# Performance work log

Hardware: AMD Instinct MI355X
Metric: run time of the kernel (lower is better)

## Reference

```python
import jax, jax.numpy as jnp
import numpy as np

B, S, D, H = 2, 2048, 1024, 16
DH = D // H
EPS = 1e-5


def _ln(x, g, b):
    m = jnp.mean(x, axis=-1, keepdims=True)
    v = jnp.mean((x - m) ** 2, axis=-1, keepdims=True)
    return (x - m) * jax.lax.rsqrt(v + EPS) * g + b


def setup_inputs() -> dict:
    key = jax.random.key(0)
    ks = jax.random.split(key, 16)
    w = lambda k, shp: jax.random.normal(k, shp, jnp.float32) * 0.02
    return {
        "x": jax.random.normal(ks[0], (B, S, D), jnp.float32),
        # semantic preprocessor: Linear(D,2D) -> ReLU -> Linear(2D,D), residual + LN
        "pW1": w(ks[1], (D, 2 * D)), "pb1": jnp.zeros((2 * D,), jnp.float32),
        "pW2": w(ks[2], (2 * D, D)), "pb2": jnp.zeros((D,), jnp.float32),
        "gp": jnp.ones((D,), jnp.float32), "bp": jnp.zeros((D,), jnp.float32),
        # multi-head attention projections
        "Wq": w(ks[3], (D, D)), "bq": jnp.zeros((D,), jnp.float32),
        "Wk": w(ks[4], (D, D)), "bk": jnp.zeros((D,), jnp.float32),
        "Wv": w(ks[5], (D, D)), "bv": jnp.zeros((D,), jnp.float32),
        "Wo": w(ks[6], (D, D)), "bo": jnp.zeros((D,), jnp.float32),
        "g1": jnp.ones((D,), jnp.float32), "b1": jnp.zeros((D,), jnp.float32),
        # FFN: Linear(D,4D) -> ReLU -> Linear(4D,D)
        "Wf1": w(ks[7], (D, 4 * D)), "bf1": jnp.zeros((4 * D,), jnp.float32),
        "Wf2": w(ks[8], (4 * D, D)), "bf2": jnp.zeros((D,), jnp.float32),
        "g2": jnp.ones((D,), jnp.float32), "b2": jnp.zeros((D,), jnp.float32),
    }


def reference(x, pW1, pb1, pW2, pb2, gp, bp,
              Wq, bq, Wk, bk, Wv, bv, Wo, bo, g1, b1,
              Wf1, bf1, Wf2, bf2, g2, b2):
    # specialized 'semantic' preprocessor (dropout = identity in eval)
    h = jax.nn.relu(x @ pW1 + pb1) @ pW2 + pb2
    s = _ln(x + h, gp, bp)                       # [B,S,D]
    # naive multi-head attention
    q = (s @ Wq + bq).reshape(B, S, H, DH)
    k = (s @ Wk + bk).reshape(B, S, H, DH)
    v = (s @ Wv + bv).reshape(B, S, H, DH)
    scores = jnp.einsum("bqhd,bkhd->bhqk", q, k) / np.sqrt(DH).astype(np.float32)
    attn = jax.nn.softmax(scores, axis=-1)       # [B,H,S,S]
    ctx = jnp.einsum("bhqk,bkhd->bqhd", attn, v).reshape(B, S, D)
    attn_out = ctx @ Wo + bo
    y = _ln(s + attn_out, g1, b1)
    # FFN (dropouts = identity)
    f = jax.nn.relu(y @ Wf1 + bf1) @ Wf2 + bf2
    return _ln(y + f, g2, b2)
```

## Files before the change

kernel.cpp:

```cpp
#include <hip/hip_runtime.h>
#include <cstdint>
#include <cstddef>

typedef _Float16 f16;
typedef _Float16 f16x8 __attribute__((ext_vector_type(8)));
typedef _Float16 f16x4 __attribute__((ext_vector_type(4)));
typedef float    f32x4 __attribute__((ext_vector_type(4)));
typedef float    f32x16 __attribute__((ext_vector_type(16)));
typedef unsigned int uint2v __attribute__((ext_vector_type(2)));

#define MFMA16(a,b,c) __builtin_amdgcn_mfma_f32_16x16x32_f16(a, b, c, 0, 0, 0)
#define MFMA32(a,b,c) __builtin_amdgcn_mfma_f32_32x32x16_f16(a, b, c, 0, 0, 0)

static __device__ __forceinline__ void gload_lds16(const void* g, void* l) {
  __builtin_amdgcn_global_load_lds(
      (const __attribute__((address_space(1))) unsigned int*)g,
      (__attribute__((address_space(3))) unsigned int*)l, 16, 0, 0);
}

static __device__ __forceinline__ int pkh(float a, float b) {
  auto t = __builtin_amdgcn_cvt_pkrtz(a, b);
  return __builtin_bit_cast(int, t);
}

static __device__ __forceinline__ float ex2(float x) {
  return __builtin_amdgcn_exp2f(x);
}

static __device__ __forceinline__ uint2v pswap(int a, int b) {
  return __builtin_amdgcn_permlane32_swap((unsigned)a, (unsigned)b, false, false);
}
static __device__ __forceinline__ float xhalf_max(float x) {
  uint2v r = pswap(__builtin_bit_cast(int, x), __builtin_bit_cast(int, x));
  return fmaxf(__builtin_bit_cast(float, r.x), __builtin_bit_cast(float, r.y));
}
static __device__ __forceinline__ float f3(float a, float b, float c) {
  return fmaxf(fmaxf(a, b), c);
}

static __device__ __forceinline__ void wtrans_blk(float (*tile)[33],
                                                  const float* __restrict__ W,
                                                  f16* __restrict__ Wt,
                                                  int K, int N, int gx,
                                                  float scale, int lb) {
  const int n0 = (lb % gx) * 32, k0 = (lb / gx) * 32;
  const int c = threadIdx.x & 31, r = threadIdx.x >> 5;
#pragma unroll
  for (int i = 0; i < 4; i++) {
    int row = r + i * 8;
    tile[row][c] = W[(size_t)(k0 + row) * N + n0 + c];
  }
  __syncthreads();
#pragma unroll
  for (int i = 0; i < 4; i++) {
    int row = r + i * 8;
    Wt[(size_t)(n0 + row) * K + k0 + c] = (f16)(tile[c][row] * scale);
  }
}

__global__ __launch_bounds__(256)
void prep_kernel(const float* __restrict__ x, f16* __restrict__ xb,
                 const float* __restrict__ pW1, f16* __restrict__ wtP1,
                 const float* __restrict__ pW2, f16* __restrict__ wtP2,
                 const float* __restrict__ Wq,  f16* __restrict__ wtQ,
                 const float* __restrict__ Wk,  f16* __restrict__ wtK,
                 const float* __restrict__ Wv,  f16* __restrict__ wtV,
                 const float* __restrict__ Wo,  f16* __restrict__ wtO,
                 const float* __restrict__ Wf1, f16* __restrict__ wtF1,
                 const float* __restrict__ Wf2, f16* __restrict__ wtF2,
                 const float* __restrict__ bq, const float* __restrict__ bk,
                 const float* __restrict__ bv, float* __restrict__ bqkv) {
  __shared__ float tile[32][33];
  int b = blockIdx.x;
  if (b < 4096) {
    int i = b * 256 + threadIdx.x;
    float4 v = ((const float4*)x)[i];
    f16x4 h;
    h[0] = (f16)v.x; h[1] = (f16)v.y; h[2] = (f16)v.z; h[3] = (f16)v.w;
    *(f16x4*)(xb + (size_t)i * 4) = h;
    return;
  }
  b -= 4096;
  if (b < 2048) { wtrans_blk(tile, pW1, wtP1, 1024, 2048, 64, 1.f, b); return; }
  b -= 2048;
  if (b < 2048) { wtrans_blk(tile, pW2, wtP2, 2048, 1024, 32, 1.f, b); return; }
  b -= 2048;
  if (b < 1024) { wtrans_blk(tile, Wq, wtQ, 1024, 1024, 32, 0.18033688f, b); return; }
  b -= 1024;
  if (b < 1024) { wtrans_blk(tile, Wk, wtK, 1024, 1024, 32, 1.f, b); return; }
  b -= 1024;
  if (b < 1024) { wtrans_blk(tile, Wv, wtV, 1024, 1024, 32, 1.f, b); return; }
  b -= 1024;
  if (b < 1024) { wtrans_blk(tile, Wo, wtO, 1024, 1024, 32, 1.f, b); return; }
  b -= 1024;
  if (b < 4096) { wtrans_blk(tile, Wf1, wtF1, 1024, 4096, 128, 1.f, b); return; }
  b -= 4096;
  if (b < 4096) { wtrans_blk(tile, Wf2, wtF2, 4096, 1024, 32, 1.f, b); return; }
  b -= 4096;
  {
    int i = b * 256 + threadIdx.x;
    if (i < 1024)       bqkv[i] = bq[i] * 0.18033688f;
    else if (i < 2048)  bqkv[i] = bk[i - 1024];
    else if (i < 3072)  bqkv[i] = bv[i - 2048];
  }
}

template <int MODE>
__global__ __launch_bounds__(256, 2)
void gemm_kernel(const f16* __restrict__ A, const f16* __restrict__ W,
                 const float* __restrict__ bias, void* __restrict__ out,
                 f16* __restrict__ vt, int N, int K, int gx) {
  __shared__ __align__(16) f16 lsA[128 * 64];
  __shared__ __align__(16) f16 lsB[128 * 64];
  const int tid  = threadIdx.x;
  const int lane = tid & 63;
  const int wid  = tid >> 6;
  const int frow = lane & 15;
  const int kgrp = lane >> 4;
  const int wmBase = (wid >> 1) * 64;
  const int wnBase = (wid & 1) * 64;

  const int bid = blockIdx.x;
  const int xcd = bid & 7, slot = bid >> 3;
  const int bm = (xcd << 2) + slot / gx;
  const int bn = slot % gx;

  const f32x4 zero4 = {0.f, 0.f, 0.f, 0.f};
  f32x4 acc[4][4];
#pragma unroll
  for (int i = 0; i < 4; i++)
#pragma unroll
    for (int j = 0; j < 4; j++) acc[i][j] = zero4;

  const f16* aSrc[4]; int lOffA[4];
  const f16* bSrc[4];
#pragma unroll
  for (int i = 0; i < 4; i++) {
    int c_lin = i * 256 + wid * 64 + lane;
    int row = c_lin >> 3;
    int ch  = (c_lin & 7) ^ (row & 7);
    aSrc[i] = A + (size_t)(bm * 128 + row) * K + ch * 8;
    bSrc[i] = W + (size_t)(bn * 128 + row) * K + ch * 8;
    lOffA[i] = (i * 256 + wid * 64) * 8;
  }

  const int nk = K >> 6;
  for (int ks = 0; ks < nk; ++ks) {
#pragma unroll
    for (int i = 0; i < 4; i++) gload_lds16(aSrc[i] + ks * 64, &lsA[lOffA[i]]);
#pragma unroll
    for (int i = 0; i < 4; i++) gload_lds16(bSrc[i] + ks * 64, &lsB[lOffA[i]]);
    __syncthreads();
#pragma unroll
    for (int kk = 0; kk < 2; kk++) {
      f16x8 af[4], bf[4];
#pragma unroll
      for (int i = 0; i < 4; i++) {
        int row = wmBase + i * 16 + frow;
        af[i] = *(const f16x8*)&lsA[row * 64 + (((kk * 4 + kgrp) ^ (row & 7)) << 3)];
      }
#pragma unroll
      for (int j = 0; j < 4; j++) {
        int row = wnBase + j * 16 + frow;
        bf[j] = *(const f16x8*)&lsB[row * 64 + (((kk * 4 + kgrp) ^ (row & 7)) << 3)];
      }
#pragma unroll
      for (int i = 0; i < 4; i++)
#pragma unroll
        for (int j = 0; j < 4; j++) acc[i][j] = MFMA16(af[i], bf[j], acc[i][j]);
    }
    __syncthreads();
  }

#pragma unroll
  for (int j = 0; j < 4; j++) {
    const int col = bn * 128 + wnBase + j * 16 + frow;
    const float bb = bias[col];
#pragma unroll
    for (int i = 0; i < 4; i++) {
      const int row0 = bm * 128 + wmBase + i * 16 + kgrp * 4;
      if (MODE == 3 && col >= 2048) {
        const int vcol = col - 2048;
        const int bh = (row0 >> 11) * 16 + (vcol >> 6);
        const int d  = vcol & 63;
        const int kv = row0 & 2047;
        f16x4 pk;
#pragma unroll
        for (int r = 0; r < 4; r++) pk[r] = (f16)(acc[i][j][r] + bb);
        *(f16x4*)(vt + ((size_t)bh * 64 + d) * 2048 + kv) = pk;
      } else {
#pragma unroll
        for (int r = 0; r < 4; r++) {
          float v = acc[i][j][r] + bb;
          if (MODE == 1) v = fmaxf(v, 0.f);
          ((f16*)out)[(size_t)(row0 + r) * N + col] = (f16)v;
        }
      }
    }
  }
}

__global__ __launch_bounds__(256, 2)
void gemm_splitk(const f16* __restrict__ A, const f16* __restrict__ W,
                 f16* __restrict__ outp, int K) {
  __shared__ __align__(16) f16 lsA[128 * 64];
  __shared__ __align__(16) f16 lsB[128 * 64];
  const int tid  = threadIdx.x;
  const int lane = tid & 63;
  const int wid  = tid >> 6;
  const int frow = lane & 15;
  const int kgrp = lane >> 4;
  const int wmBase = (wid >> 1) * 64;
  const int wnBase = (wid & 1) * 64;

  const int bid = blockIdx.x;
  const int xcd = bid & 7, slot = bid >> 3;
  const int q = slot >> 3, bn = slot & 7;
  const int bmkp = xcd * 8 + q;
  const int bm = bmkp >> 1, kp = bmkp & 1;
  const int Kh = K >> 1;
  const f16* Ab = A + kp * Kh;
  const f16* Wb = W + kp * Kh;

  const f32x4 zero4 = {0.f, 0.f, 0.f, 0.f};
  f32x4 acc[4][4];
#pragma unroll
  for (int i = 0; i < 4; i++)
#pragma unroll
    for (int j = 0; j < 4; j++) acc[i][j] = zero4;

  const f16* aSrc[4]; const f16* bSrc[4]; int lOff[4];
#pragma unroll
  for (int i = 0; i < 4; i++) {
    int c_lin = i * 256 + wid * 64 + lane;
    int row = c_lin >> 3;
    int ch  = (c_lin & 7) ^ (row & 7);
    aSrc[i] = Ab + (size_t)(bm * 128 + row) * K + ch * 8;
    bSrc[i] = Wb + (size_t)(bn * 128 + row) * K + ch * 8;
    lOff[i] = (i * 256 + wid * 64) * 8;
  }

  const int nk = Kh >> 6;
  for (int ks = 0; ks < nk; ++ks) {
#pragma unroll
    for (int i = 0; i < 4; i++) gload_lds16(aSrc[i] + ks * 64, &lsA[lOff[i]]);
#pragma unroll
    for (int i = 0; i < 4; i++) gload_lds16(bSrc[i] + ks * 64, &lsB[lOff[i]]);
    __syncthreads();
#pragma unroll
    for (int kk = 0; kk < 2; kk++) {
      f16x8 af[4], bf[4];
#pragma unroll
      for (int i = 0; i < 4; i++) {
        int row = wmBase + i * 16 + frow;
        af[i] = *(const f16x8*)&lsA[row * 64 + (((kk * 4 + kgrp) ^ (row & 7)) << 3)];
      }
#pragma unroll
      for (int j = 0; j < 4; j++) {
        int row = wnBase + j * 16 + frow;
        bf[j] = *(const f16x8*)&lsB[row * 64 + (((kk * 4 + kgrp) ^ (row & 7)) << 3)];
      }
#pragma unroll
      for (int i = 0; i < 4; i++)
#pragma unroll
        for (int j = 0; j < 4; j++) acc[i][j] = MFMA16(af[i], bf[j], acc[i][j]);
    }
    __syncthreads();
  }

  f16* op = outp + (size_t)kp * 4096 * 1024;
#pragma unroll
  for (int j = 0; j < 4; j++) {
    const int col = bn * 128 + wnBase + j * 16 + frow;
#pragma unroll
    for (int i = 0; i < 4; i++) {
      const int row0 = bm * 128 + wmBase + i * 16 + kgrp * 4;
#pragma unroll
      for (int r = 0; r < 4; r++)
        op[(size_t)(row0 + r) * 1024 + col] = (f16)acc[i][j][r];
    }
  }
}

__global__ __launch_bounds__(256)
void ln_res2(const f16* __restrict__ p, const f16* __restrict__ res,
             const float* __restrict__ bias, const float* __restrict__ g,
             const float* __restrict__ be, float* __restrict__ of,
             f16* __restrict__ ob) {
  const int row = blockIdx.x, t = threadIdx.x;
  const size_t off = (size_t)row * 1024 + t * 4;
  const f16x4 a = *(const f16x4*)(p + off);
  const f16x4 b = *(const f16x4*)(p + (size_t)4096 * 1024 + off);
  const f16x4 rr = *(const f16x4*)(res + off);
  const float4 bb = ((const float4*)bias)[t];
  float v0 = (float)a[0] + (float)b[0] + bb.x + (float)rr[0];
  float v1 = (float)a[1] + (float)b[1] + bb.y + (float)rr[1];
  float v2 = (float)a[2] + (float)b[2] + bb.z + (float)rr[2];
  float v3 = (float)a[3] + (float)b[3] + bb.w + (float)rr[3];
  float s = v0 + v1 + v2 + v3;
  float q = v0 * v0 + v1 * v1 + v2 * v2 + v3 * v3;
#pragma unroll
  for (int o = 1; o < 64; o <<= 1) {
    s += __shfl_xor(s, o);
    q += __shfl_xor(q, o);
  }
  __shared__ float ss[4], sq[4];
  if ((t & 63) == 0) { ss[t >> 6] = s; sq[t >> 6] = q; }
  __syncthreads();
  s = ss[0] + ss[1] + ss[2] + ss[3];
  q = sq[0] + sq[1] + sq[2] + sq[3];
  const float mean = s * (1.f / 1024.f);
  const float var  = q * (1.f / 1024.f) - mean * mean;
  const float rstd = rsqrtf(var + 1e-5f);
  const float4 gv = ((const float4*)g)[t];
  const float4 bv = ((const float4*)be)[t];
  float4 ov;
  ov.x = (v0 - mean) * rstd * gv.x + bv.x;
  ov.y = (v1 - mean) * rstd * gv.y + bv.y;
  ov.z = (v2 - mean) * rstd * gv.z + bv.z;
  ov.w = (v3 - mean) * rstd * gv.w + bv.w;
  if (of) ((float4*)(of + (size_t)row * 1024))[t] = ov;
  if (ob) {
    f16x4 hv;
    hv[0] = (f16)ov.x; hv[1] = (f16)ov.y; hv[2] = (f16)ov.z; hv[3] = (f16)ov.w;
    *(f16x4*)(ob + off) = hv;
  }
}

__global__ __launch_bounds__(256, 4)
void attn_kernel(const f16* __restrict__ Qp, const f16* __restrict__ Kp,
                 const f16* __restrict__ Vt, f16* __restrict__ opart,
                 float* __restrict__ Lbuf, int ldq) {
  __shared__ __align__(16) f16 lsKb[2 * 64 * 64];
  __shared__ __align__(16) f16 lsVb[2 * 64 * 64];
  const int tid = threadIdx.x, lane = tid & 63, wid = tid >> 6;
  const int qcol = lane & 31;
  const int hi = lane >> 5;
  const int bid = blockIdx.x;
  const int idx = bid >> 3;
  const int bh = ((bid & 7) << 2) | (idx & 3);
  const int rest = idx >> 2;
  const int part = rest & 1;
  const int qt = rest >> 1;
  const int b = bh >> 4, h = bh & 15;
  const size_t rb = (size_t)b * 2048;
  const int hc = h * 64;
  const int kv0 = part * 1024;
  const int qrow = qt * 128 + wid * 32 + qcol;

  f16x8 qf[4];
  {
    const f16* qp = Qp + (rb + qrow) * ldq + hc;
#pragma unroll
    for (int kc = 0; kc < 4; kc++) qf[kc] = *(const f16x8*)(qp + kc * 16 + hi * 8);
  }
  f16x8 ones;
#pragma unroll
  for (int i = 0; i < 8; i++) ones[i] = (f16)1.0f;

  f32x16 ot0, ot1, lacc;
#pragma unroll
  for (int i = 0; i < 16; i++) { ot0[i] = 0.f; ot1[i] = 0.f; lacc[i] = 0.f; }
  float mrun = -1e30f;

  const f16 *kS0, *kS1, *vS0, *vS1;
  int off0, off1;
  {
    int c0 = wid * 64 + lane;
    int r0 = c0 >> 3, ch0 = (c0 & 7) ^ (r0 & 7);
    int c1 = 256 + wid * 64 + lane;
    int r1 = c1 >> 3, ch1 = (c1 & 7) ^ (r1 & 7);
    kS0 = Kp + (rb + kv0 + r0) * ldq + hc + ch0 * 8;
    kS1 = Kp + (rb + kv0 + r1) * ldq + hc + ch1 * 8;
    const f16* vbase = Vt + (size_t)bh * 64 * 2048 + kv0;
    vS0 = vbase + (size_t)r0 * 2048 + ch0 * 8;
    vS1 = vbase + (size_t)r1 * 2048 + ch1 * 8;
    off0 = (wid * 64) * 8;
    off1 = (256 + wid * 64) * 8;
  }

#define ASTAGE(T, PB)                                                    \
  {                                                                      \
    f16* kd = lsKb + (PB) * 4096;                                        \
    f16* vd = lsVb + (PB) * 4096;                                        \
    const size_t ko = (size_t)(T) * 64 * ldq;                            \
    const size_t vo = (size_t)(T) * 64;                                  \
    gload_lds16(kS0 + ko, kd + off0);                                    \
    gload_lds16(kS1 + ko, kd + off1);                                    \
    gload_lds16(vS0 + vo, vd + off0);                                    \
    gload_lds16(vS1 + vo, vd + off1);                                    \
  }

  ASTAGE(0, 0);
  asm volatile("s_waitcnt vmcnt(0)" ::: "memory");
  __builtin_amdgcn_s_barrier();

  for (int kt = 0; kt < 16; ++kt) {
    const int cur = kt & 1;
    if (kt < 15) ASTAGE(kt + 1, cur ^ 1);
    const f16* kb = lsKb + cur * 4096;
    const f16* vb = lsVb + cur * 4096;

    f32x16 s0, s1;
#pragma unroll
    for (int i = 0; i < 16; i++) { s0[i] = 0.f; s1[i] = 0.f; }
    const int kr0 = qcol, kr1 = 32 + qcol;
    __builtin_amdgcn_s_setprio(1);
#pragma unroll
    for (int kc = 0; kc < 4; kc++) {
      f16x8 a0 = *(const f16x8*)&kb[kr0 * 64 + (((kc * 2 + hi) ^ (kr0 & 7)) << 3)];
      f16x8 a1 = *(const f16x8*)&kb[kr1 * 64 + (((kc * 2 + hi) ^ (kr1 & 7)) << 3)];
      s0 = MFMA32(a0, qf[kc], s0);
      s1 = MFMA32(a1, qf[kc], s1);
    }
    __builtin_amdgcn_s_setprio(0);

    float t10[11];
#pragma unroll
    for (int r = 0; r < 10; r++) {
      float e0 = (3 * r + 0 < 16) ? s0[(3 * r + 0) & 15] : s1[(3 * r + 0) & 15];
      float e1 = (3 * r + 1 < 16) ? s0[(3 * r + 1) & 15] : s1[(3 * r + 1) & 15];
      float e2 = (3 * r + 2 < 16) ? s0[(3 * r + 2) & 15] : s1[(3 * r + 2) & 15];
      t10[r] = f3(e0, e1, e2);
    }
    t10[10] = fmaxf(s1[14], s1[15]);
    float p0 = f3(t10[0], t10[1], t10[2]);
    float p1 = f3(t10[3], t10[4], t10[5]);
    float p2 = f3(t10[6], t10[7], t10[8]);
    float p3 = fmaxf(t10[9], t10[10]);
    float pmax = xhalf_max(fmaxf(fmaxf(p0, p1), fmaxf(p2, p3)));
    if (__any(pmax > mrun + 11.54f)) {
      float mn = fmaxf(mrun, pmax);
      float fac = ex2(mrun - mn);
      mrun = mn;
#pragma unroll
      for (int i = 0; i < 16; i++) {
        ot0[i] *= fac; ot1[i] *= fac; lacc[i] *= fac;
      }
    }
#pragma unroll
    for (int r = 0; r < 16; r++) {
      s0[r] = ex2(s0[r] - mrun);
      s1[r] = ex2(s1[r] - mrun);
    }

#pragma unroll
    for (int st = 0; st < 2; ++st) {
#pragma unroll
      for (int c0 = 0; c0 < 2; c0++) {
        const int c8 = c0 * 8;
        int a0, a1, b0, b1;
        if (st == 0) {
          a0 = pkh(s0[c8 + 0], s0[c8 + 1]); a1 = pkh(s0[c8 + 2], s0[c8 + 3]);
          b0 = pkh(s0[c8 + 4], s0[c8 + 5]); b1 = pkh(s0[c8 + 6], s0[c8 + 7]);
        } else {
          a0 = pkh(s1[c8 + 0], s1[c8 + 1]); a1 = pkh(s1[c8 + 2], s1[c8 + 3]);
          b0 = pkh(s1[c8 + 4], s1[c8 + 5]); b1 = pkh(s1[c8 + 6], s1[c8 + 7]);
        }
        uint2v r0 = pswap(a0, b0);
        uint2v r1 = pswap(a1, b1);
        int4 wv;
        wv.x = (int)r0.x; wv.y = (int)r1.x; wv.z = (int)r0.y; wv.w = (int)r1.y;
        f16x8 pfrag = __builtin_bit_cast(f16x8, wv);
        const int ch = st * 4 + c0 * 2 + hi;
        const int vr0 = qcol, vr1 = 32 + qcol;
        f16x8 av0 = *(const f16x8*)&vb[vr0 * 64 + ((ch ^ (vr0 & 7)) << 3)];
        f16x8 av1 = *(const f16x8*)&vb[vr1 * 64 + ((ch ^ (vr1 & 7)) << 3)];
        __builtin_amdgcn_s_setprio(1);
        ot0 = MFMA32(av0, pfrag, ot0);
        ot1 = MFMA32(av1, pfrag, ot1);
        lacc = MFMA32(ones, pfrag, lacc);
        __builtin_amdgcn_s_setprio(0);
      }
    }
    asm volatile("s_waitcnt vmcnt(0)" ::: "memory");
    __builtin_amdgcn_s_barrier();
  }
#undef ASTAGE

  const float lfin = lacc[0];
  const float rinv = 1.f / lfin;
  const size_t pbase = ((size_t)part * 32 + bh) * 2048 + qrow;
  f16* pp = opart + pbase * 64;
#pragma unroll
  for (int rr = 0; rr < 16; rr += 2) {
    const int d = (rr & 3) + 8 * (rr >> 2) + 4 * hi;
    *(int*)(pp + d)      = pkh(ot0[rr] * rinv, ot0[rr + 1] * rinv);
    *(int*)(pp + 32 + d) = pkh(ot1[rr] * rinv, ot1[rr + 1] * rinv);
  }
  if (hi == 0) Lbuf[pbase] = mrun + __builtin_amdgcn_logf(lfin);
}

__global__ __launch_bounds__(256)
void combine_kernel(const f16* __restrict__ opart, const float* __restrict__ Lbuf,
                    f16* __restrict__ ctx) {
  const int bid = blockIdx.x;
  const int bh = bid >> 5, qblk = bid & 31;
  const int t = threadIdx.x;
  const int q = qblk * 64 + (t >> 2);
  const int dp = (t & 3) * 16;
  const size_t base = (size_t)bh * 2048 + q;
  const size_t p1o = (size_t)32 * 2048;
  const float L0 = Lbuf[base];
  const float L1 = Lbuf[p1o + base];
  const float L = fmaxf(L0, L1);
  float w0 = ex2(L0 - L), w1 = ex2(L1 - L);
  const float rs = 1.f / (w0 + w1);
  w0 *= rs; w1 *= rs;
  const f16* p0 = opart + base * 64 + dp;
  const f16* p1 = opart + (p1o + base) * 64 + dp;
  f16x8 a0 = *(const f16x8*)p0, a1 = *(const f16x8*)(p0 + 8);
  f16x8 c0 = *(const f16x8*)p1, c1 = *(const f16x8*)(p1 + 8);
  f16x8 o0, o1;
#pragma unroll
  for (int j = 0; j < 8; j++) {
    o0[j] = (f16)(w0 * (float)a0[j] + w1 * (float)c0[j]);
    o1[j] = (f16)(w0 * (float)a1[j] + w1 * (float)c1[j]);
  }
  const int b = bh >> 4, h = bh & 15;
  f16* op = ctx + ((size_t)b * 2048 + q) * 1024 + h * 64 + dp;
  *(f16x8*)op = o0;
  *(f16x8*)(op + 8) = o1;
}

extern "C" void kernel_launch(void* const* d_in, const int* in_sizes, int n_in,
                              void* d_out, int out_size, void* d_ws, size_t ws_size,
                              hipStream_t stream) {
  const float* x   = (const float*)d_in[0];
  const float* pW1 = (const float*)d_in[1];
  const float* pb1 = (const float*)d_in[2];
  const float* pW2 = (const float*)d_in[3];
  const float* pb2 = (const float*)d_in[4];
  const float* gp  = (const float*)d_in[5];
  const float* bp  = (const float*)d_in[6];
  const float* Wq  = (const float*)d_in[7];
  const float* bq  = (const float*)d_in[8];
  const float* Wk  = (const float*)d_in[9];
  const float* bk  = (const float*)d_in[10];
  const float* Wv  = (const float*)d_in[11];
  const float* bv  = (const float*)d_in[12];
  const float* Wo  = (const float*)d_in[13];
  const float* bo  = (const float*)d_in[14];
  const float* g1  = (const float*)d_in[15];
  const float* b1  = (const float*)d_in[16];
  const float* Wf1 = (const float*)d_in[17];
  const float* bf1 = (const float*)d_in[18];
  const float* Wf2 = (const float*)d_in[19];
  const float* bf2 = (const float*)d_in[20];
  const float* g2  = (const float*)d_in[21];
  const float* b2  = (const float*)d_in[22];

  char* ws = (char*)d_ws;
  const size_t MB = 1024 * 1024;
  if (ws_size < 121 * MB) return;

  f16*   wtP1 = (f16*)(ws);
  f16*   wtP2 = (f16*)(ws + 4 * MB);
  f16*   wtQ  = (f16*)(ws + 8 * MB);
  f16*   wtO  = (f16*)(ws + 14 * MB);
  f16*   wtF1 = (f16*)(ws + 16 * MB);
  f16*   wtF2 = (f16*)(ws + 24 * MB);
  f16*   big  = (f16*)(ws + 32 * MB);
  f16*   xb   = (f16*)(ws + 64 * MB);
  f16*   sb   = (f16*)(ws + 72 * MB);
  f16*   ybuf = (f16*)(ws + 80 * MB);
  f16*   ctx  = (f16*)(ws + 88 * MB);
  f16*   part = (f16*)(ws + 96 * MB);
  f16*   opart= (f16*)(ws + 96 * MB);
  float* Lbuf = (float*)(ws + 112 * MB);
  float* bqkv = (float*)(ws + 112 * MB + 512 * 1024);
  f16*   wtK  = wtQ + (size_t)1024 * 1024;
  f16*   wtV  = wtQ + (size_t)2048 * 1024;
  f16*   Vt   = big + (size_t)4096 * 3072;

  dim3 blk(256);
  prep_kernel<<<20492, blk, 0, stream>>>(x, xb, pW1, wtP1, pW2, wtP2,
                                         Wq, wtQ, Wk, wtK, Wv, wtV, Wo, wtO,
                                         Wf1, wtF1, Wf2, wtF2, bq, bk, bv, bqkv);

  gemm_kernel<1><<<512, blk, 0, stream>>>(xb, wtP1, pb1, big, nullptr, 2048, 1024, 16);
  gemm_splitk<<<512, blk, 0, stream>>>(big, wtP2, part, 2048);
  ln_res2<<<4096, blk, 0, stream>>>(part, xb, pb2, gp, bp, nullptr, sb);
  gemm_kernel<3><<<768, blk, 0, stream>>>(sb, wtQ, bqkv, big, Vt, 3072, 1024, 24);
  attn_kernel<<<1024, blk, 0, stream>>>(big, big + 1024, Vt, opart, Lbuf, 3072);
  combine_kernel<<<1024, blk, 0, stream>>>(opart, Lbuf, ctx);
  gemm_splitk<<<512, blk, 0, stream>>>(ctx, wtO, part, 1024);
  ln_res2<<<4096, blk, 0, stream>>>(part, sb, bo, g1, b1, nullptr, ybuf);
  gemm_kernel<1><<<1024, blk, 0, stream>>>(ybuf, wtF1, bf1, big, nullptr, 4096, 1024, 32);
  gemm_splitk<<<512, blk, 0, stream>>>(big, wtF2, part, 4096);
  ln_res2<<<4096, blk, 0, stream>>>(part, ybuf, bf2, g2, b2, (float*)d_out, nullptr);
}
```

Measured before the change: 272.3 us.

## Double-buffer LDS tiles in split-K and first GEMM to overlap loads with MFMA

```diff
diff --git a/kernel.cpp b/kernel.cpp
--- a/kernel.cpp
+++ b/kernel.cpp
@@ -105,13 +105,14 @@
   }
 }
 
-template <int MODE>
+template <int MODE, bool PF>
 __global__ __launch_bounds__(256, 2)
 void gemm_kernel(const f16* __restrict__ A, const f16* __restrict__ W,
                  const float* __restrict__ bias, void* __restrict__ out,
                  f16* __restrict__ vt, int N, int K, int gx) {
-  __shared__ __align__(16) f16 lsA[128 * 64];
-  __shared__ __align__(16) f16 lsB[128 * 64];
+  constexpr int BUFS = PF ? 2 : 1;
+  __shared__ __align__(16) f16 lsA[BUFS * 128 * 64];
+  __shared__ __align__(16) f16 lsB[BUFS * 128 * 64];
   const int tid  = threadIdx.x;
   const int lane = tid & 63;
   const int wid  = tid >> 6;
@@ -144,32 +145,60 @@
     lOffA[i] = (i * 256 + wid * 64) * 8;
   }
 
-  const int nk = K >> 6;
-  for (int ks = 0; ks < nk; ++ks) {
-#pragma unroll
-    for (int i = 0; i < 4; i++) gload_lds16(aSrc[i] + ks * 64, &lsA[lOffA[i]]);
-#pragma unroll
-    for (int i = 0; i < 4; i++) gload_lds16(bSrc[i] + ks * 64, &lsB[lOffA[i]]);
-    __syncthreads();
+  auto compute = [&](const f16* la, const f16* lb) {
 #pragma unroll
     for (int kk = 0; kk < 2; kk++) {
       f16x8 af[4], bf[4];
 #pragma unroll
       for (int i = 0; i < 4; i++) {
         int row = wmBase + i * 16 + frow;
-        af[i] = *(const f16x8*)&lsA[row * 64 + (((kk * 4 + kgrp) ^ (row & 7)) << 3)];
+        af[i] = *(const f16x8*)&la[row * 64 + (((kk * 4 + kgrp) ^ (row & 7)) << 3)];
       }
 #pragma unroll
       for (int j = 0; j < 4; j++) {
         int row = wnBase + j * 16 + frow;
-        bf[j] = *(const f16x8*)&lsB[row * 64 + (((kk * 4 + kgrp) ^ (row & 7)) << 3)];
+        bf[j] = *(const f16x8*)&lb[row * 64 + (((kk * 4 + kgrp) ^ (row & 7)) << 3)];
       }
 #pragma unroll
       for (int i = 0; i < 4; i++)
 #pragma unroll
         for (int j = 0; j < 4; j++) acc[i][j] = MFMA16(af[i], bf[j], acc[i][j]);
     }
-    __syncthreads();
+  };
+
+  const int nk = K >> 6;
+  if constexpr (PF) {
+#define GST(T, PB)                                                        \
+    {                                                                     \
+      f16* la = lsA + (PB) * 8192;                                        \
+      f16* lb = lsB + (PB) * 8192;                                        \
+      _Pragma("unroll") for (int i = 0; i < 4; i++) {                     \
+        gload_lds16(aSrc[i] + (size_t)(T) * 64, la + lOffA[i]);           \
+        gload_lds16(bSrc[i] + (size_t)(T) * 64, lb + lOffA[i]);           \
+      }                                                                   \
+    }
+    GST(0, 0);
+    for (int ks = 0; ks < nk; ++ks) {
+      const int nt = (ks + 1 < nk) ? ks + 1 : nk - 1;
+      GST(nt, (ks + 1) & 1);
+      asm volatile("s_waitcnt vmcnt(8)" ::: "memory");
+      __builtin_amdgcn_s_barrier();
+      compute(lsA + (ks & 1) * 8192, lsB + (ks & 1) * 8192);
+      __builtin_amdgcn_s_barrier();
+    }
+    asm volatile("s_waitcnt vmcnt(0)" ::: "memory");
+#undef GST
+  } else {
+    for (int ks = 0; ks < nk; ++ks) {
+#pragma unroll
+      for (int i = 0; i < 4; i++) {
+        gload_lds16(aSrc[i] + (size_t)ks * 64, &lsA[lOffA[i]]);
+        gload_lds16(bSrc[i] + (size_t)ks * 64, &lsB[lOffA[i]]);
+      }
+      __syncthreads();
+      compute(lsA, lsB);
+      __syncthreads();
+    }
   }
 
 #pragma unroll
@@ -203,8 +232,8 @@
 __global__ __launch_bounds__(256, 2)
 void gemm_splitk(const f16* __restrict__ A, const f16* __restrict__ W,
                  f16* __restrict__ outp, int K) {
-  __shared__ __align__(16) f16 lsA[128 * 64];
-  __shared__ __align__(16) f16 lsB[128 * 64];
+  __shared__ __align__(16) f16 lsA[2 * 128 * 64];
+  __shared__ __align__(16) f16 lsB[2 * 128 * 64];
   const int tid  = threadIdx.x;
   const int lane = tid & 63;
   const int wid  = tid >> 6;
@@ -240,33 +269,48 @@
     lOff[i] = (i * 256 + wid * 64) * 8;
   }
 
-  const int nk = Kh >> 6;
-  for (int ks = 0; ks < nk; ++ks) {
-#pragma unroll
-    for (int i = 0; i < 4; i++) gload_lds16(aSrc[i] + ks * 64, &lsA[lOff[i]]);
-#pragma unroll
-    for (int i = 0; i < 4; i++) gload_lds16(bSrc[i] + ks * 64, &lsB[lOff[i]]);
-    __syncthreads();
+  auto compute = [&](const f16* la, const f16* lb) {
 #pragma unroll
     for (int kk = 0; kk < 2; kk++) {
       f16x8 af[4], bf[4];
 #pragma unroll
       for (int i = 0; i < 4; i++) {
         int row = wmBase + i * 16 + frow;
-        af[i] = *(const f16x8*)&lsA[row * 64 + (((kk * 4 + kgrp) ^ (row & 7)) << 3)];
+        af[i] = *(const f16x8*)&la[row * 64 + (((kk * 4 + kgrp) ^ (row & 7)) << 3)];
       }
 #pragma unroll
       for (int j = 0; j < 4; j++) {
         int row = wnBase + j * 16 + frow;
-        bf[j] = *(const f16x8*)&lsB[row * 64 + (((kk * 4 + kgrp) ^ (row & 7)) << 3)];
+        bf[j] = *(const f16x8*)&lb[row * 64 + (((kk * 4 + kgrp) ^ (row & 7)) << 3)];
       }
 #pragma unroll
       for (int i = 0; i < 4; i++)
 #pragma unroll
         for (int j = 0; j < 4; j++) acc[i][j] = MFMA16(af[i], bf[j], acc[i][j]);
     }
-    __syncthreads();
-  }
+  };
+
+#define GST(T, PB)                                                        \
+  {                                                                       \
+    f16* la = lsA + (PB) * 8192;                                          \
+    f16* lb = lsB + (PB) * 8192;                                          \
+    _Pragma("unroll") for (int i = 0; i < 4; i++) {                       \
+      gload_lds16(aSrc[i] + (size_t)(T) * 64, la + lOff[i]);              \
+      gload_lds16(bSrc[i] + (size_t)(T) * 64, lb + lOff[i]);              \
+    }                                                                     \
+  }
+  const int nk = Kh >> 6;
+  GST(0, 0);
+  for (int ks = 0; ks < nk; ++ks) {
+    const int nt = (ks + 1 < nk) ? ks + 1 : nk - 1;
+    GST(nt, (ks + 1) & 1);
+    asm volatile("s_waitcnt vmcnt(8)" ::: "memory");
+    __builtin_amdgcn_s_barrier();
+    compute(lsA + (ks & 1) * 8192, lsB + (ks & 1) * 8192);
+    __builtin_amdgcn_s_barrier();
+  }
+  asm volatile("s_waitcnt vmcnt(0)" ::: "memory");
+#undef GST
 
   f16* op = outp + (size_t)kp * 4096 * 1024;
 #pragma unroll
@@ -578,15 +622,15 @@
                                          Wq, wtQ, Wk, wtK, Wv, wtV, Wo, wtO,
                                          Wf1, wtF1, Wf2, wtF2, bq, bk, bv, bqkv);
 
-  gemm_kernel<1><<<512, blk, 0, stream>>>(xb, wtP1, pb1, big, nullptr, 2048, 1024, 16);
+  gemm_kernel<1, true><<<512, blk, 0, stream>>>(xb, wtP1, pb1, big, nullptr, 2048, 1024, 16);
   gemm_splitk<<<512, blk, 0, stream>>>(big, wtP2, part, 2048);
   ln_res2<<<4096, blk, 0, stream>>>(part, xb, pb2, gp, bp, nullptr, sb);
-  gemm_kernel<3><<<768, blk, 0, stream>>>(sb, wtQ, bqkv, big, Vt, 3072, 1024, 24);
+  gemm_kernel<3, false><<<768, blk, 0, stream>>>(sb, wtQ, bqkv, big, Vt, 3072, 1024, 24);
   attn_kernel<<<1024, blk, 0, stream>>>(big, big + 1024, Vt, opart, Lbuf, 3072);
   combine_kernel<<<1024, blk, 0, stream>>>(opart, Lbuf, ctx);
   gemm_splitk<<<512, blk, 0, stream>>>(ctx, wtO, part, 1024);
   ln_res2<<<4096, blk, 0, stream>>>(part, sb, bo, g1, b1, nullptr, ybuf);
-  gemm_kernel<1><<<1024, blk, 0, stream>>>(ybuf, wtF1, bf1, big, nullptr, 4096, 1024, 32);
+  gemm_kernel<1, false><<<1024, blk, 0, stream>>>(ybuf, wtF1, bf1, big, nullptr, 4096, 1024, 32);
   gemm_splitk<<<512, blk, 0, stream>>>(big, wtF2, part, 4096);
   ln_res2<<<4096, blk, 0, stream>>>(part, ybuf, bf2, g2, b2, (float*)d_out, nullptr);
 }
```

Result: no change. 271.5 us, median of 2 (-0.3%).
